# Optimization experiments

Hardware: AMD Instinct MI355X
Metric: run time of the kernel (lower is better)

The kernel has to match this reference:

```python
import jax, jax.numpy as jnp
import numpy as np

DIM = 1024
LN_EPS = 1e-5

def _layernorm(x, w, b):
    m = jnp.mean(x, axis=-1, keepdims=True)
    v = jnp.mean((x - m) ** 2, axis=-1, keepdims=True)
    return (x - m) * jax.lax.rsqrt(v + LN_EPS) * w + b

def _linear(x, w, b):
    # torch Linear: w is (out, in)
    return jnp.einsum('bsd,od->bso', x, w) + b

def setup_inputs() -> dict:
    key = jax.random.key(0)
    ks = jax.random.split(key, 8)
    d = DIM
    s = 0.02
    return {
        'x': jax.random.normal(ks[0], (4, 4096, d), dtype=jnp.float32),
        'ln1_w': jnp.ones((d,), jnp.float32), 'ln1_b': jnp.zeros((d,), jnp.float32),
        'ln2_w': jnp.ones((d,), jnp.float32), 'ln2_b': jnp.zeros((d,), jnp.float32),
        'gate_w': jax.random.normal(ks[1], (d, d), jnp.float32) * s,
        'gate_b': jnp.zeros((d,), jnp.float32),
        'val_w': jax.random.normal(ks[2], (d, d), jnp.float32) * s,
        'val_b': jnp.zeros((d,), jnp.float32),
        'ffn1_w': jax.random.normal(ks[3], (4 * d, d), jnp.float32) * s,
        'ffn1_b': jnp.zeros((4 * d,), jnp.float32),
        'ffn2_w': jax.random.normal(ks[4], (d, 4 * d), jnp.float32) * s,
        'ffn2_b': jnp.zeros((d,), jnp.float32),
    }

def reference(x, ln1_w, ln1_b, ln2_w, ln2_b, gate_w, gate_b, val_w, val_b, ffn1_w, ffn1_b, ffn2_w, ffn2_b):
    batch, seq_len, dim = x.shape
    h = _layernorm(x, ln1_w, ln1_b)
    g = jax.nn.sigmoid(_linear(h, gate_w, gate_b))
    v = _linear(h, val_w, val_b)
    cumsum_v = jnp.cumsum(g * v, axis=1)
    cumsum_g = jnp.cumsum(g, axis=1) + 1e-6
    position = jnp.arange(1, seq_len + 1, dtype=x.dtype)[None, :, None]  # [1,S,1]
    mem = cumsum_v / (jnp.sqrt(cumsum_g) * jnp.sqrt(position / seq_len + 0.1))
    x = x + mem
    h2 = _layernorm(x, ln2_w, ln2_b)
    ff = _linear(jax.nn.gelu(_linear(h2, ffn1_w, ffn1_b), approximate=False), ffn2_w, ffn2_b)
    return x + ff
```

## Files before the change

### kernel.cpp

```cpp
#include <hip/hip_runtime.h>
#include <cstdint>
#include <cstddef>

#define DIMD 1024
#define SEQ  4096
#define BATCH 4
#define MTOT (BATCH*SEQ)
#define NCHUNK 64
#define CLEN   64

typedef __attribute__((ext_vector_type(8))) short short8;
typedef __attribute__((ext_vector_type(4))) float floatx4;

__device__ __forceinline__ unsigned short f2bf(float f){
  unsigned u = __float_as_uint(f);
  u += 0x7fffu + ((u >> 16) & 1u);
  return (unsigned short)(u >> 16);
}
__device__ __forceinline__ float bf2f(unsigned short u){
  return __uint_as_float((unsigned)u << 16);
}

__device__ __forceinline__ void async16(const void* g, void* l){
  __builtin_amdgcn_global_load_lds(
      (const __attribute__((address_space(1))) void*)g,
      (__attribute__((address_space(3))) void*)l, 16, 0, 0);
}

__global__ void f32_to_bf16_kernel(const float* __restrict__ in,
                                   unsigned short* __restrict__ out, int n){
  int i = (blockIdx.x * 256 + threadIdx.x) * 4;
  if (i < n){
    float4 v = *(const float4*)(in + i);
    uint2 o;
    o.x = (unsigned)f2bf(v.x) | ((unsigned)f2bf(v.y) << 16);
    o.y = (unsigned)f2bf(v.z) | ((unsigned)f2bf(v.w) << 16);
    *(uint2*)(out + i) = o;
  }
}

__global__ __launch_bounds__(256)
void ln_kernel(const float* __restrict__ X, const float* __restrict__ w,
               const float* __restrict__ b, unsigned short* __restrict__ H){
  const int row = blockIdx.x;
  const int tid = threadIdx.x;
  const float4 xv = ((const float4*)(X + (size_t)row * DIMD))[tid];
  float s  = xv.x + xv.y + xv.z + xv.w;
  float ss = xv.x*xv.x + xv.y*xv.y + xv.z*xv.z + xv.w*xv.w;
  #pragma unroll
  for (int o = 32; o; o >>= 1){
    s  += __shfl_down(s, o);
    ss += __shfl_down(ss, o);
  }
  __shared__ float ps[4], pss[4], mv[2];
  const int wid = tid >> 6, lane = tid & 63;
  if (lane == 0){ ps[wid] = s; pss[wid] = ss; }
  __syncthreads();
  if (tid == 0){
    float S1 = ps[0]+ps[1]+ps[2]+ps[3];
    float S2 = pss[0]+pss[1]+pss[2]+pss[3];
    float m = S1 * (1.0f / DIMD);
    float var = S2 * (1.0f / DIMD) - m*m;
    mv[0] = m; mv[1] = rsqrtf(var + 1e-5f);
  }
  __syncthreads();
  const float m = mv[0], rs = mv[1];
  const float4 wv = ((const float4*)w)[tid];
  const float4 bv = ((const float4*)b)[tid];
  float o0 = (xv.x - m) * rs * wv.x + bv.x;
  float o1 = (xv.y - m) * rs * wv.y + bv.y;
  float o2 = (xv.z - m) * rs * wv.z + bv.z;
  float o3 = (xv.w - m) * rs * wv.w + bv.w;
  uint2 o;
  o.x = (unsigned)f2bf(o0) | ((unsigned)f2bf(o1) << 16);
  o.y = (unsigned)f2bf(o2) | ((unsigned)f2bf(o3) << 16);
  ((uint2*)(H + (size_t)row * DIMD))[tid] = o;
}

template<int EPI>
__global__ __launch_bounds__(256, 3)
void gemm_bf16(const unsigned short* __restrict__ A, int lda,
               const unsigned short* __restrict__ Bw, int ldb,
               const float* __restrict__ bias, const float* __restrict__ bias2,
               void* __restrict__ OutP, void* __restrict__ Out2P,
               int ldc, int grid_n, int K)
{
  __shared__ unsigned short Alds[2][128*32];
  __shared__ unsigned short Blds[2][128*32];
  __shared__ char slab[4][4096];
  const int tid = threadIdx.x;
  const int bid = ((int)blockIdx.x & 7) * ((int)gridDim.x >> 3) + ((int)blockIdx.x >> 3);
  const int bm = bid / grid_n, bn = bid % grid_n;
  const int row0 = bm * 128, col0 = bn * 128;
  const int wid = tid >> 6, lane = tid & 63;
  const int wr = wid >> 1, wc = wid & 1;
  const int l15 = lane & 15, kh = (lane >> 4) * 8, rq = lane >> 4;

  const int idx0 = tid * 8;
  const int idx1 = 2048 + tid * 8;
  const int ar0 = idx0 >> 5, ac0 = idx0 & 31;
  const int ar1 = idx1 >> 5, ac1 = idx1 & 31;

  floatx4 acc[4][4];
  #pragma unroll
  for (int m = 0; m < 4; ++m)
    #pragma unroll
    for (int n = 0; n < 4; ++n)
      acc[m][n] = (floatx4){0.f, 0.f, 0.f, 0.f};

  auto stage = [&](int b, int k0){
    async16(A  + (size_t)(row0 + ar0) * lda + k0 + ac0, (char*)(&Alds[b][0]) + idx0*2);
    async16(A  + (size_t)(row0 + ar1) * lda + k0 + ac1, (char*)(&Alds[b][0]) + idx1*2);
    async16(Bw + (size_t)(col0 + ar0) * ldb + k0 + ac0, (char*)(&Blds[b][0]) + idx0*2);
    async16(Bw + (size_t)(col0 + ar1) * ldb + k0 + ac1, (char*)(&Blds[b][0]) + idx1*2);
  };
  auto compute = [&](int b){
    short8 af[4], bfr[4];
    #pragma unroll
    for (int m = 0; m < 4; ++m)
      af[m] = *(const short8*)(&Alds[b][(wr*64 + m*16 + l15)*32 + kh]);
    #pragma unroll
    for (int n = 0; n < 4; ++n)
      bfr[n] = *(const short8*)(&Blds[b][(wc*64 + n*16 + l15)*32 + kh]);
    #pragma unroll
    for (int m = 0; m < 4; ++m)
      #pragma unroll
      for (int n = 0; n < 4; ++n)
        acc[m][n] = __builtin_amdgcn_mfma_f32_16x16x32_bf16(af[m], bfr[n], acc[m][n], 0, 0, 0);
  };

  const int nt = K >> 5;
  stage(0, 0);
  __syncthreads();
  int cur = 0;
  for (int t = 0; t < nt - 1; ++t){
    stage(cur ^ 1, (t + 1) << 5);
    compute(cur);
    __syncthreads();
    cur ^= 1;
  }
  compute(cur);

  if constexpr (EPI == 2 || EPI == 5){
    __syncthreads();
    char* sl = &slab[wid][0];
    unsigned short* dst; int colw; int ldout; bool sigm = false;
    const float* bsel;
    if constexpr (EPI == 5){
      const int c0 = col0 + wc * 64;
      if (c0 < 1024){ dst = (unsigned short*)OutP;  colw = c0;        bsel = bias;  sigm = true;  }
      else          { dst = (unsigned short*)Out2P; colw = c0 - 1024; bsel = bias2; sigm = false; }
      ldout = 1024;
    } else {
      dst = (unsigned short*)OutP; colw = col0 + wc * 64; bsel = bias; ldout = ldc;
    }
    const int rdrow = lane >> 3;
    const int rdoff  = rdrow * 128 + (((lane & 7) ^ (rdrow & 7)) << 4);
    const int rdoff2 = (rdrow + 8) * 128 + (((lane & 7) ^ ((rdrow + 8) & 7)) << 4);
    const int rdsl = (lane & 7) * 16;
    #pragma unroll
    for (int m = 0; m < 4; ++m){
      #pragma unroll
      for (int n = 0; n < 4; ++n){
        const float bs = bsel[colw + n*16 + l15];
        const int cchunk = n*2 + (l15 >> 3);
        #pragma unroll
        for (int j = 0; j < 4; ++j){
          const float val = acc[m][n][j] + bs;
          float r;
          if constexpr (EPI == 2){
            r = 0.5f * val * (1.f + erff(val * 0.70710678118f));
          } else {
            r = sigm ? (1.f / (1.f + expf(-val))) : val;
          }
          const int rr = rq*4 + j;
          *(unsigned short*)(sl + rr*128 + ((cchunk ^ (rr & 7)) << 4) + (l15 & 7)*2) = f2bf(r);
        }
      }
      asm volatile("s_waitcnt lgkmcnt(0)" ::: "memory");
      uint4 w0 = *(const uint4*)(sl + rdoff);
      uint4 w1 = *(const uint4*)(sl + rdoff2);
      asm volatile("s_waitcnt lgkmcnt(0)" ::: "memory");
      const int growb = row0 + wr * 64 + m * 16;
      *(uint4*)((char*)(dst + (size_t)(growb + rdrow) * ldout + colw) + rdsl) = w0;
      *(uint4*)((char*)(dst + (size_t)(growb + rdrow + 8) * ldout + colw) + rdsl) = w1;
    }
  } else {
    #pragma unroll
    for (int n = 0; n < 4; ++n){
      const int col = col0 + wc * 64 + n * 16 + l15;
      const float bs = (EPI == 4) ? 0.f : bias[col];
      #pragma unroll
      for (int m = 0; m < 4; ++m){
        const int rowb = row0 + wr * 64 + m * 16 + rq * 4;
        #pragma unroll
        for (int j = 0; j < 4; ++j){
          const size_t o = (size_t)(rowb + j) * ldc + col;
          float* O = (float*)OutP;
          O[o] = acc[m][n][j] + bs + O[o];
        }
      }
    }
  }
}

__global__ __launch_bounds__(256)
void scan_sums(const unsigned short* __restrict__ G, const unsigned short* __restrict__ V,
               float* __restrict__ SG, float* __restrict__ SGV){
  const int bc = blockIdx.x;
  const int d  = blockIdx.y * 256 + threadIdx.x;
  const int b = bc >> 6, c = bc & 63;
  size_t base = ((size_t)b * SEQ + (size_t)c * CLEN) * DIMD + d;
  float sg = 0.f, sgv = 0.f;
  for (int i = 0; i < CLEN; ++i){
    float g = bf2f(G[base + (size_t)i * DIMD]);
    float v = bf2f(V[base + (size_t)i * DIMD]);
    sg += g; sgv += g * v;
  }
  SG[(size_t)bc * DIMD + d] = sg;
  SGV[(size_t)bc * DIMD + d] = sgv;
}

__global__ __launch_bounds__(256)
void scan_prefix(float* __restrict__ SG, float* __restrict__ SGV){
  const int b = blockIdx.x;
  const int d = blockIdx.y * 256 + threadIdx.x;
  float rg = 0.f, rgv = 0.f;
  for (int c = 0; c < NCHUNK; ++c){
    size_t i = ((size_t)(b * NCHUNK + c)) * DIMD + d;
    float tg = SG[i], tv = SGV[i];
    SG[i] = rg; SGV[i] = rgv;
    rg += tg; rgv += tv;
  }
}

__global__ __launch_bounds__(256)
void scan_final(const unsigned short* __restrict__ G, const unsigned short* __restrict__ V,
                const float* __restrict__ SG, const float* __restrict__ SGV,
                const float* __restrict__ X, float* __restrict__ X2){
  const int bc = blockIdx.x;
  const int d  = blockIdx.y * 256 + threadIdx.x;
  const int b = bc >> 6, c = bc & 63;
  size_t base = ((size_t)b * SEQ + (size_t)c * CLEN) * DIMD + d;
  float rg  = SG[(size_t)bc * DIMD + d];
  float rgv = SGV[(size_t)bc * DIMD + d];
  for (int i = 0; i < CLEN; ++i){
    size_t idx = base + (size_t)i * DIMD;
    float g = bf2f(G[idx]), v = bf2f(V[idx]);
    rg += g; rgv += g * v;
    int s = c * CLEN + i;
    float pf = (float)(s + 1) * (1.0f / SEQ) + 0.1f;
    float mem = rgv * rsqrtf((rg + 1e-6f) * pf);
    X2[idx] = X[idx] + mem;
  }
}

extern "C" void kernel_launch(void* const* d_in, const int* in_sizes, int n_in,
                              void* d_out, int out_size, void* d_ws, size_t ws_size,
                              hipStream_t stream)
{
  const float* x     = (const float*)d_in[0];
  const float* ln1w  = (const float*)d_in[1];
  const float* ln1b  = (const float*)d_in[2];
  const float* ln2w  = (const float*)d_in[3];
  const float* ln2b  = (const float*)d_in[4];
  const float* gatew = (const float*)d_in[5];
  const float* gateb = (const float*)d_in[6];
  const float* valw  = (const float*)d_in[7];
  const float* valb  = (const float*)d_in[8];
  const float* f1w   = (const float*)d_in[9];
  const float* f1b   = (const float*)d_in[10];
  const float* f2w   = (const float*)d_in[11];
  const float* f2b   = (const float*)d_in[12];
  float* out = (float*)d_out;

  const size_t MB = 1024u * 1024u;
  const size_t baseNeed = (size_t)(32+32+32+2+2+8+8)*MB + 2u*BATCH*NCHUNK*DIMD*4 + 4096;
  const bool bigT = (baseNeed + 64u*MB) <= ws_size;

  char* ws = (char*)d_ws;
  size_t off = 0;
  auto alloc = [&](size_t bytes) -> char* {
    char* p = ws + off; off += (bytes + 255) & ~(size_t)255; return p;
  };
  unsigned short* H  = (unsigned short*)alloc((size_t)MTOT * DIMD * 2);
  unsigned short* G  = (unsigned short*)alloc((size_t)MTOT * DIMD * 2);
  unsigned short* V  = (unsigned short*)alloc((size_t)MTOT * DIMD * 2);
  if (bigT) alloc(64u * MB);
  unsigned short* T  = G;
  unsigned short* WGV= (unsigned short*)alloc((size_t)2 * DIMD * DIMD * 2);
  unsigned short* W1 = (unsigned short*)alloc((size_t)4 * DIMD * DIMD * 2);
  unsigned short* W2 = (unsigned short*)alloc((size_t)4 * DIMD * DIMD * 2);
  float* SG  = (float*)alloc((size_t)BATCH * NCHUNK * DIMD * 4);
  float* SGV = (float*)alloc((size_t)BATCH * NCHUNK * DIMD * 4);

  if (off > ws_size) return;

  f32_to_bf16_kernel<<<DIMD*DIMD/1024, 256, 0, stream>>>(gatew, WGV, DIMD*DIMD);
  f32_to_bf16_kernel<<<DIMD*DIMD/1024, 256, 0, stream>>>(valw,  WGV + (size_t)DIMD*DIMD, DIMD*DIMD);
  f32_to_bf16_kernel<<<4*DIMD*DIMD/1024, 256, 0, stream>>>(f1w, W1, 4*DIMD*DIMD);
  f32_to_bf16_kernel<<<4*DIMD*DIMD/1024, 256, 0, stream>>>(f2w, W2, 4*DIMD*DIMD);

  ln_kernel<<<MTOT, 256, 0, stream>>>(x, ln1w, ln1b, H);

  gemm_bf16<5><<<(MTOT/128)*(2048/128), 256, 0, stream>>>(
      H, DIMD, WGV, DIMD, gateb, valb, G, V, 2048, 2048/128, DIMD);

  scan_sums  <<<dim3(BATCH*NCHUNK, DIMD/256), 256, 0, stream>>>(G, V, SG, SGV);
  scan_prefix<<<dim3(BATCH, DIMD/256),        256, 0, stream>>>(SG, SGV);
  scan_final <<<dim3(BATCH*NCHUNK, DIMD/256), 256, 0, stream>>>(G, V, SG, SGV, x, out);

  ln_kernel<<<MTOT, 256, 0, stream>>>(out, ln2w, ln2b, H);

  if (bigT){
    gemm_bf16<2><<<(MTOT/128)*(4096/128), 256, 0, stream>>>(
        H, DIMD, W1, DIMD, f1b, nullptr, T, nullptr, 4*DIMD, 4096/128, DIMD);
    gemm_bf16<3><<<(MTOT/128)*(DIMD/128), 256, 0, stream>>>(
        T, 4*DIMD, W2, 4*DIMD, f2b, nullptr, out, nullptr, DIMD, DIMD/128, 4*DIMD);
  } else {
    for (int c = 0; c < 2; ++c){
      const unsigned short* W1c = W1 + (size_t)c * 2048 * DIMD;
      const unsigned short* W2c = W2 + (size_t)c * 2048;
      gemm_bf16<2><<<(MTOT/128)*(2048/128), 256, 0, stream>>>(
          H, DIMD, W1c, DIMD, f1b + c*2048, nullptr, T, nullptr, 2048, 2048/128, DIMD);
      if (c == 0)
        gemm_bf16<3><<<(MTOT/128)*(DIMD/128), 256, 0, stream>>>(
            T, 2048, W2c, 4*DIMD, f2b, nullptr, out, nullptr, DIMD, DIMD/128, 2048);
      else
        gemm_bf16<4><<<(MTOT/128)*(DIMD/128), 256, 0, stream>>>(
            T, 2048, W2c, 4*DIMD, nullptr, nullptr, out, nullptr, DIMD, DIMD/128, 2048);
    }
  }
}
```

Baseline: 599.0 us.

## Swizzle GEMM LDS layout, use fast sigmoid/tanh-GELU, split FFN1 launches

Rewrites the GEMM staging so each thread loads a swizzled 16-byte slot per row, with XOR-swizzled LDS read offsets precomputed per fragment. This is meant to cut LDS bank conflicts and per-iteration address arithmetic. It also replaces exact erf GELU and expf sigmoid with a tanh-style GELU approximation built on hardware exp2/rcp, which changes numerics slightly. It drops the occupancy hint from launch bounds and a barrier before the epilogue, and splits the big FFN1 GEMM into two column-half launches.

```diff
diff --git a/kernel.cpp b/kernel.cpp
--- a/kernel.cpp
+++ b/kernel.cpp
@@ -19,6 +19,14 @@
 }
 __device__ __forceinline__ float bf2f(unsigned short u){
   return __uint_as_float((unsigned)u << 16);
+}
+
+__device__ __forceinline__ float fast_sigmoid(float x){
+  return __builtin_amdgcn_rcpf(1.f + __builtin_amdgcn_exp2f(-1.442695041f * x));
+}
+__device__ __forceinline__ float fast_gelu(float x){
+  float u = 1.595769122f * x * (1.f + 0.044715f * x * x);
+  return x * fast_sigmoid(u);
 }
 
 __device__ __forceinline__ void async16(const void* g, void* l){
@@ -78,12 +86,12 @@
 }
 
 template<int EPI>
-__global__ __launch_bounds__(256, 3)
-void gemm_bf16(const unsigned short* __restrict__ A, int lda,
-               const unsigned short* __restrict__ Bw, int ldb,
-               const float* __restrict__ bias, const float* __restrict__ bias2,
-               void* __restrict__ OutP, void* __restrict__ Out2P,
-               int ldc, int grid_n, int K)
+__global__ __launch_bounds__(256)
+void gemm128(const unsigned short* __restrict__ A, int lda,
+             const unsigned short* __restrict__ Bw, int ldb,
+             const float* __restrict__ bias, const float* __restrict__ bias2,
+             void* __restrict__ OutP, void* __restrict__ Out2P,
+             int ldc, int grid_n, int K)
 {
   __shared__ unsigned short Alds[2][128*32];
   __shared__ unsigned short Blds[2][128*32];
@@ -94,12 +102,25 @@
   const int row0 = bm * 128, col0 = bn * 128;
   const int wid = tid >> 6, lane = tid & 63;
   const int wr = wid >> 1, wc = wid & 1;
-  const int l15 = lane & 15, kh = (lane >> 4) * 8, rq = lane >> 4;
-
-  const int idx0 = tid * 8;
-  const int idx1 = 2048 + tid * 8;
-  const int ar0 = idx0 >> 5, ac0 = idx0 & 31;
-  const int ar1 = idx1 >> 5, ac1 = idx1 & 31;
+  const int l15 = lane & 15, rq = lane >> 4;
+
+  const int st_sl = (tid & 3) ^ ((tid >> 3) & 3);
+  const unsigned short* aP = A  + (size_t)(row0 + (tid >> 2)) * lda + st_sl * 8;
+  const unsigned short* bP = Bw + (size_t)(col0 + (tid >> 2)) * ldb + st_sl * 8;
+  const int st_off = tid * 16;
+  const size_t lda64 = (size_t)lda * 64, ldb64 = (size_t)ldb * 64;
+
+  int offA[4], offB[4];
+  #pragma unroll
+  for (int m = 0; m < 4; ++m){
+    const int r = wr*64 + m*16 + l15;
+    offA[m] = r*64 + ((rq ^ ((r >> 1) & 3)) << 4);
+  }
+  #pragma unroll
+  for (int n = 0; n < 4; ++n){
+    const int r = wc*64 + n*16 + l15;
+    offB[n] = r*64 + ((rq ^ ((r >> 1) & 3)) << 4);
+  }
 
   floatx4 acc[4][4];
   #pragma unroll
@@ -108,20 +129,20 @@
     for (int n = 0; n < 4; ++n)
       acc[m][n] = (floatx4){0.f, 0.f, 0.f, 0.f};
 
-  auto stage = [&](int b, int k0){
-    async16(A  + (size_t)(row0 + ar0) * lda + k0 + ac0, (char*)(&Alds[b][0]) + idx0*2);
-    async16(A  + (size_t)(row0 + ar1) * lda + k0 + ac1, (char*)(&Alds[b][0]) + idx1*2);
-    async16(Bw + (size_t)(col0 + ar0) * ldb + k0 + ac0, (char*)(&Blds[b][0]) + idx0*2);
-    async16(Bw + (size_t)(col0 + ar1) * ldb + k0 + ac1, (char*)(&Blds[b][0]) + idx1*2);
+  auto stage = [&](int b, int kel){
+    async16(aP + kel,         (char*)(&Alds[b][0]) + st_off);
+    async16(aP + lda64 + kel, (char*)(&Alds[b][0]) + 4096 + st_off);
+    async16(bP + kel,         (char*)(&Blds[b][0]) + st_off);
+    async16(bP + ldb64 + kel, (char*)(&Blds[b][0]) + 4096 + st_off);
   };
   auto compute = [&](int b){
     short8 af[4], bfr[4];
     #pragma unroll
     for (int m = 0; m < 4; ++m)
-      af[m] = *(const short8*)(&Alds[b][(wr*64 + m*16 + l15)*32 + kh]);
+      af[m] = *(const short8*)((const char*)(&Alds[b][0]) + offA[m]);
     #pragma unroll
     for (int n = 0; n < 4; ++n)
-      bfr[n] = *(const short8*)(&Blds[b][(wc*64 + n*16 + l15)*32 + kh]);
+      bfr[n] = *(const short8*)((const char*)(&Blds[b][0]) + offB[n]);
     #pragma unroll
     for (int m = 0; m < 4; ++m)
       #pragma unroll
@@ -142,7 +163,6 @@
   compute(cur);
 
   if constexpr (EPI == 2 || EPI == 5){
-    __syncthreads();
     char* sl = &slab[wid][0];
     unsigned short* dst; int colw; int ldout; bool sigm = false;
     const float* bsel;
@@ -169,9 +189,9 @@
           const float val = acc[m][n][j] + bs;
           float r;
           if constexpr (EPI == 2){
-            r = 0.5f * val * (1.f + erff(val * 0.70710678118f));
+            r = fast_gelu(val);
           } else {
-            r = sigm ? (1.f / (1.f + expf(-val))) : val;
+            r = sigm ? fast_sigmoid(val) : val;
           }
           const int rr = rq*4 + j;
           *(unsigned short*)(sl + rr*128 + ((cchunk ^ (rr & 7)) << 4) + (l15 & 7)*2) = f2bf(r);
@@ -303,7 +323,7 @@
 
   ln_kernel<<<MTOT, 256, 0, stream>>>(x, ln1w, ln1b, H);
 
-  gemm_bf16<5><<<(MTOT/128)*(2048/128), 256, 0, stream>>>(
+  gemm128<5><<<(MTOT/128)*(2048/128), 256, 0, stream>>>(
       H, DIMD, WGV, DIMD, gateb, valb, G, V, 2048, 2048/128, DIMD);
 
   scan_sums  <<<dim3(BATCH*NCHUNK, DIMD/256), 256, 0, stream>>>(G, V, SG, SGV);
@@ -313,21 +333,23 @@
   ln_kernel<<<MTOT, 256, 0, stream>>>(out, ln2w, ln2b, H);
 
   if (bigT){
-    gemm_bf16<2><<<(MTOT/128)*(4096/128), 256, 0, stream>>>(
-        H, DIMD, W1, DIMD, f1b, nullptr, T, nullptr, 4*DIMD, 4096/128, DIMD);
-    gemm_bf16<3><<<(MTOT/128)*(DIMD/128), 256, 0, stream>>>(
+    for (int c = 0; c < 2; ++c)
+      gemm128<2><<<(MTOT/128)*(2048/128), 256, 0, stream>>>(
+          H, DIMD, W1 + (size_t)c*2048*DIMD, DIMD, f1b + c*2048, nullptr,
+          T + (size_t)c*2048, nullptr, 4*DIMD, 2048/128, DIMD);
+    gemm128<3><<<(MTOT/128)*(DIMD/128), 256, 0, stream>>>(
         T, 4*DIMD, W2, 4*DIMD, f2b, nullptr, out, nullptr, DIMD, DIMD/128, 4*DIMD);
   } else {
     for (int c = 0; c < 2; ++c){
       const unsigned short* W1c = W1 + (size_t)c * 2048 * DIMD;
       const unsigned short* W2c = W2 + (size_t)c * 2048;
-      gemm_bf16<2><<<(MTOT/128)*(2048/128), 256, 0, stream>>>(
+      gemm128<2><<<(MTOT/128)*(2048/128), 256, 0, stream>>>(
           H, DIMD, W1c, DIMD, f1b + c*2048, nullptr, T, nullptr, 2048, 2048/128, DIMD);
       if (c == 0)
-        gemm_bf16<3><<<(MTOT/128)*(DIMD/128), 256, 0, stream>>>(
+        gemm128<3><<<(MTOT/128)*(DIMD/128), 256, 0, stream>>>(
             T, 2048, W2c, 4*DIMD, f2b, nullptr, out, nullptr, DIMD, DIMD/128, 2048);
       else
-        gemm_bf16<4><<<(MTOT/128)*(DIMD/128), 256, 0, stream>>>(
+        gemm128<4><<<(MTOT/128)*(DIMD/128), 256, 0, stream>>>(
             T, 2048, W2c, 4*DIMD, nullptr, nullptr, out, nullptr, DIMD, DIMD/128, 2048);
     }
   }
```

After: 636.9 us. +6.3%, slower.
